# Kernel optimization log

Hardware: AMD Instinct MI355X
Metric: run time of the kernel (lower is better)

The kernel has to match this reference:

```python
import jax, jax.numpy as jnp
import numpy as np

DIM = 2048
HID = 1024
E = 16
TOP_K = 2
S_SHARED = 2


def setup_inputs() -> dict:
    key = jax.random.key(0)
    ks = jax.random.split(key, 6)
    scale = 0.02
    x = jax.random.normal(ks[0], (2, 2048, DIM), dtype=jnp.float32)
    gate_w = jax.random.normal(ks[1], (DIM, E), dtype=jnp.float32) * scale
    shared_w1 = jax.random.normal(ks[2], (S_SHARED, DIM, HID), dtype=jnp.float32) * scale
    shared_w2 = jax.random.normal(ks[3], (S_SHARED, HID, DIM), dtype=jnp.float32) * scale
    w1 = jax.random.normal(ks[4], (E, DIM, HID), dtype=jnp.float32) * scale
    w2 = jax.random.normal(ks[5], (E, HID, DIM), dtype=jnp.float32) * scale
    return {"x": x, "gate_w": gate_w, "shared_w1": shared_w1,
            "shared_w2": shared_w2, "w1": w1, "w2": w2}


def reference(x, gate_w, shared_w1, shared_w2, w1, w2):
    orig_shape = x.shape
    xf = x.reshape(-1, orig_shape[-1])  # [T, D]

    # Shared experts: sum of SiLU MLPs
    hs = jax.nn.silu(jnp.einsum('td,sdh->sth', xf, shared_w1))
    shared_out = jnp.einsum('sth,shd->td', hs, shared_w2)

    # Gating
    probs = jax.nn.softmax(xf @ gate_w, axis=-1)              # [T, E]
    weights, indices = jax.lax.top_k(probs, TOP_K)            # [T, K]
    weights = weights / weights.sum(axis=-1, keepdims=True)
    aux_loss = (probs.mean(axis=0) ** 2).sum() * E

    # Combine weights per (token, expert): top_k indices are distinct
    combine = (jax.nn.one_hot(indices, E, dtype=xf.dtype) *
               weights[..., None]).sum(axis=1)                # [T, E]

    # Dense all-expert compute (reference form of gather-GEMM-scatter)
    h = jax.nn.silu(jnp.einsum('td,edh->eth', xf, w1))        # [E, T, H]
    y = jnp.einsum('eth,ehd->etd', h, w2)                     # [E, T, D]
    routed_out = jnp.einsum('te,etd->td', combine, y)         # [T, D]

    out = (shared_out + routed_out).reshape(orig_shape)
    return out, aux_loss
```

## Files before the change

### kernel.cpp

```cpp
#include <hip/hip_runtime.h>
#include <math.h>

typedef unsigned short u16;
typedef __bf16 bf16x8 __attribute__((ext_vector_type(8)));
typedef float f32x4 __attribute__((ext_vector_type(4)));
typedef unsigned short u16x8 __attribute__((ext_vector_type(8)));

#define T_TOK 4096
#define DIMD 2048
#define HIDD 1024
#define NEXP 16
#define RMAX 10240
#define MAXBLK 96
#define BM 128
#define BN 256
#define BK 64

__device__ __forceinline__ u16 f2b(float f) {
  unsigned u = __builtin_bit_cast(unsigned, f);
  unsigned r = (u + 0x7FFFu + ((u >> 16) & 1u)) >> 16;
  return (u16)r;
}

__device__ __forceinline__ void gld16(const void* g, void* l) {
  __builtin_amdgcn_global_load_lds(
      (const __attribute__((address_space(1))) void*)g,
      (__attribute__((address_space(3))) void*)l, 16, 0, 0);
}


__global__ void k_pre(const float* __restrict__ x, u16* __restrict__ xb,
                      float* __restrict__ out, int* __restrict__ perm,
                      int* __restrict__ cnt, int* __restrict__ fill) {
  const int i = blockIdx.x * blockDim.x + threadIdx.x;
  const float4 v = ((const float4*)x)[i];
  union { u16 u[4]; unsigned long long q; } t;
  t.u[0] = f2b(v.x); t.u[1] = f2b(v.y); t.u[2] = f2b(v.z); t.u[3] = f2b(v.w);
  ((unsigned long long*)xb)[i] = t.q;
  float4 z = {0.f, 0.f, 0.f, 0.f};
  ((float4*)out)[i] = z;
  if (i < RMAX) perm[i] = -1;
  if (i < NEXP) { cnt[i] = 0; fill[i] = 0; }
}

template <int ID>
__global__ __launch_bounds__(256)
void k_tr2(const float* __restrict__ W, u16* __restrict__ Wt,
           int K, int N, long estride, int ld_out) {
  __shared__ float t[64][65];
  const int e = blockIdx.z;
  const float* Win = W + (size_t)e * (size_t)K * (size_t)N;
  u16* Wo = Wt + (size_t)e * (size_t)estride;
  const int n0 = blockIdx.x * 64, k0 = blockIdx.y * 64;
  {
    const int r = threadIdx.x >> 4;
    const int c = (threadIdx.x & 15) * 4;
#pragma unroll
    for (int p = 0; p < 4; ++p) {
      const int kk = p * 16 + r;
      const float4 v = *(const float4*)&Win[(size_t)(k0 + kk) * N + n0 + c];
      t[kk][c] = v.x; t[kk][c + 1] = v.y; t[kk][c + 2] = v.z; t[kk][c + 3] = v.w;
    }
  }
  __syncthreads();
  {
    const int r2 = threadIdx.x >> 3;
    const int g8 = (threadIdx.x & 7) * 8;
#pragma unroll
    for (int p = 0; p < 2; ++p) {
      const int nn = p * 32 + r2;
      u16x8 o;
#pragma unroll
      for (int i = 0; i < 8; ++i) o[i] = f2b(t[g8 + i][nn]);
      *(u16x8*)&Wo[(size_t)(n0 + nn) * ld_out + k0 + g8] = o;
    }
  }
}

__global__ __launch_bounds__(256)
void k_gate(const float* __restrict__ x, const float* __restrict__ gw,
            int* __restrict__ top2i, float* __restrict__ top2w,
            int* __restrict__ cnt, float* __restrict__ partial) {
  const int e = threadIdx.x & 15;
  const int tt = threadIdx.x >> 4;
  const int t = blockIdx.x * 16 + tt;
  const float* xp = x + (size_t)t * DIMD;
  float acc = 0.f;
#pragma unroll 8
  for (int k = 0; k < DIMD; ++k) acc = fmaf(xp[k], gw[k * NEXP + e], acc);
  __shared__ float lg[16][17];
  __shared__ float pr[16][17];
  lg[tt][e] = acc;
  __syncthreads();
  if (e == 0) {
    float l[16];
    float mx = -1e30f;
    for (int j = 0; j < 16; ++j) { l[j] = lg[tt][j]; mx = fmaxf(mx, l[j]); }
    float s = 0.f;
    for (int j = 0; j < 16; ++j) { l[j] = expf(l[j] - mx); s += l[j]; }
    const float inv = 1.f / s;
    float p1 = -1.f, p2 = -1.f; int i1 = 0, i2 = 0;
    for (int j = 0; j < 16; ++j) {
      const float p = l[j] * inv;
      pr[tt][j] = p;
      if (p > p1) { p2 = p1; i2 = i1; p1 = p; i1 = j; }
      else if (p > p2) { p2 = p; i2 = j; }
    }
    const float wsum = p1 + p2;
    top2i[t * 2 + 0] = i1;
    top2i[t * 2 + 1] = i2;
    top2w[t * 2 + 0] = p1 / wsum;
    top2w[t * 2 + 1] = p2 / wsum;
    atomicAdd(&cnt[i1], 1);
    atomicAdd(&cnt[i2], 1);
  }
  __syncthreads();
  if (tt == 0) {
    float s = 0.f;
    for (int j = 0; j < 16; ++j) s += pr[j][e];
    partial[blockIdx.x * 16 + e] = s;
  }
}

__global__ __launch_bounds__(256)
void k_aux(const float* __restrict__ partial, float* __restrict__ auxOut) {
  __shared__ float s[16][17];
  const int e = threadIdx.x & 15, c = threadIdx.x >> 4;
  float a = 0.f;
  for (int b = c; b < 256; b += 16) a += partial[b * 16 + e];
  s[c][e] = a;
  __syncthreads();
  if (threadIdx.x == 0) {
    float aux = 0.f;
    for (int j = 0; j < 16; ++j) {
      float tot = 0.f;
      for (int cc = 0; cc < 16; ++cc) tot += s[cc][j];
      const float m = tot / (float)T_TOK;
      aux += m * m;
    }
    auxOut[0] = aux * (float)NEXP;
  }
}

__global__ void k_off(const int* __restrict__ cnt, int* __restrict__ offs,
                      int* __restrict__ tbl_e, int* __restrict__ tbl_r0,
                      int* __restrict__ nblk) {
  if (threadIdx.x != 0 || blockIdx.x != 0) return;
  int o = 0, nb = 0;
  for (int e = 0; e < NEXP; ++e) {
    offs[e] = o;
    const int b = (cnt[e] + BM - 1) / BM;
    for (int i = 0; i < b; ++i) { tbl_e[nb] = e; tbl_r0[nb] = o + i * BM; ++nb; }
    o += b * BM;
  }
  offs[NEXP] = o;
  nblk[0] = nb;
}

__global__ void k_fill(const int* __restrict__ top2i, const float* __restrict__ top2w,
                       const int* __restrict__ offs, int* __restrict__ fill,
                       int* __restrict__ perm, float* __restrict__ wrow) {
  const int id = blockIdx.x * blockDim.x + threadIdx.x;
  if (id >= T_TOK * 2) return;
  const int e = top2i[id];
  const int pos = atomicAdd(&fill[e], 1);
  const int r = offs[e] + pos;
  perm[r] = id >> 1;
  wrow[r] = top2w[id];
}


__device__ __forceinline__ void stage_tile(
    const u16* gA0, const u16* gA1, const u16* gB0, const u16* gB1,
    const u16* gB2, const u16* gB3, int k0, u16* S, int b, int w) {
  u16* As = S + b * 24576;
  u16* Bs = As + 8192;
  gld16(gA0 + k0, As + w * 512);
  gld16(gA1 + k0, As + 4096 + w * 512);
  gld16(gB0 + k0, Bs + w * 512);
  gld16(gB1 + k0, Bs + 4096 + w * 512);
  gld16(gB2 + k0, Bs + 8192 + w * 512);
  gld16(gB3 + k0, Bs + 12288 + w * 512);
}

__device__ __forceinline__ void comp_tile(const u16* __restrict__ S, int b,
    const int (&aoff)[4][2], const int (&boff)[4][2], f32x4 (&acc)[4][4]) {
  const u16* As = S + b * 24576;
  const u16* Bs = As + 8192;
#pragma unroll
  for (int kh = 0; kh < 2; ++kh) {
    bf16x8 a[4], bq[4];
#pragma unroll
    for (int i = 0; i < 4; ++i) a[i] = *(const bf16x8*)(As + aoff[i][kh]);
#pragma unroll
    for (int j = 0; j < 4; ++j) bq[j] = *(const bf16x8*)(Bs + boff[j][kh]);
    __builtin_amdgcn_s_setprio(1);
#pragma unroll
    for (int i = 0; i < 4; ++i)
#pragma unroll
      for (int j = 0; j < 4; ++j)
        acc[i][j] = __builtin_amdgcn_mfma_f32_16x16x32_bf16(a[i], bq[j], acc[i][j], 0, 0, 0);
    __builtin_amdgcn_s_setprio(0);
  }
}

#define FENCE asm volatile("" ::: "memory")
#define VMW6  asm volatile("s_waitcnt vmcnt(6)" ::: "memory")
#define VMW0  asm volatile("s_waitcnt vmcnt(0)" ::: "memory")

__device__ __forceinline__ void gemm_pipe(
    const u16* gA0, const u16* gA1, const u16* gB0, const u16* gB1,
    const u16* gB2, const u16* gB3, int K, u16* S,
    const int (&aoff)[4][2], const int (&boff)[4][2],
    f32x4 (&acc)[4][4], int w) {
  const int nt = K >> 6;
  stage_tile(gA0, gA1, gB0, gB1, gB2, gB3, 0, S, 0, w);
  stage_tile(gA0, gA1, gB0, gB1, gB2, gB3, 64, S, 1, w);
  VMW6;
  __builtin_amdgcn_s_barrier();
  FENCE;
  for (int t = 0; t < nt - 2; ++t) {
    comp_tile(S, t & 1, aoff, boff, acc);
    FENCE;
    __builtin_amdgcn_s_barrier();
    FENCE;
    stage_tile(gA0, gA1, gB0, gB1, gB2, gB3, (t + 2) << 6, S, t & 1, w);
    VMW6;
    __builtin_amdgcn_s_barrier();
    FENCE;
  }
  comp_tile(S, 0, aoff, boff, acc);
  VMW0;
  __builtin_amdgcn_s_barrier();
  FENCE;
  comp_tile(S, 1, aoff, boff, acc);
}

__global__ __launch_bounds__(512, 2)
void k_up(const u16* __restrict__ xb, const u16* __restrict__ sw1t,
          const u16* __restrict__ w1t, u16* __restrict__ hbS,
          u16* __restrict__ hbR, const int* __restrict__ perm,
          const int* __restrict__ tbl_e, const int* __restrict__ tbl_r0,
          const int* __restrict__ nblk) {
  __shared__ u16 S[49152];
  const int bx = blockIdx.x, by = blockIdx.y;
  const int tid = threadIdx.x;
  const int w = tid >> 6, lane = tid & 63;
  const int lm = lane & 15, lq = lane >> 4;
  const int wm = w >> 2, wn = w & 3;
  const int srow = w * 8 + (lane >> 3);
  const int c8 = lane & 7;

  const bool routed = bx >= 32;
  int r0, ga0, ga1;
  const u16* Bb;
  if (!routed) {
    r0 = bx * BM;
    Bb = sw1t;
    ga0 = r0 + srow; ga1 = r0 + 64 + srow;
  } else {
    if (by >= 4) return;
    const int rbx = bx - 32;
    if (rbx >= *nblk) return;
    const int e = tbl_e[rbx];
    r0 = tbl_r0[rbx];
    Bb = w1t + (size_t)e * (size_t)HIDD * DIMD;
    const int p0 = perm[r0 + srow];      ga0 = (p0 < 0) ? 0 : p0;
    const int p1 = perm[r0 + 64 + srow]; ga1 = (p1 < 0) ? 0 : p1;
  }
  const int n0 = by * BN;
  const u16* gA0 = xb + (size_t)ga0 * DIMD + (c8 ^ ((srow >> 1) & 7)) * 8;
  const u16* gA1 = xb + (size_t)ga1 * DIMD + (c8 ^ (((64 + srow) >> 1) & 7)) * 8;
  const u16* gB[4];
#pragma unroll
  for (int p = 0; p < 4; ++p) {
    const int n = p * 64 + srow;
    gB[p] = Bb + (size_t)(n0 + n) * DIMD + (c8 ^ ((n >> 1) & 7)) * 8;
  }
  int aoff[4][2], boff[4][2];
#pragma unroll
  for (int i = 0; i < 4; ++i) {
    const int m = wm * 64 + i * 16 + lm;
    const int n = wn * 64 + i * 16 + lm;
#pragma unroll
    for (int kh = 0; kh < 2; ++kh) {
      aoff[i][kh] = m * 64 + (((kh << 2) | lq) ^ ((m >> 1) & 7)) * 8;
      boff[i][kh] = n * 64 + (((kh << 2) | lq) ^ ((n >> 1) & 7)) * 8;
    }
  }
  f32x4 acc[4][4];
#pragma unroll
  for (int i = 0; i < 4; ++i)
#pragma unroll
    for (int j = 0; j < 4; ++j) {
      acc[i][j][0] = 0.f; acc[i][j][1] = 0.f; acc[i][j][2] = 0.f; acc[i][j][3] = 0.f;
    }

  gemm_pipe(gA0, gA1, gB[0], gB[1], gB[2], gB[3], DIMD, S, aoff, boff, acc, w);

#pragma unroll
  for (int i = 0; i < 4; ++i) {
#pragma unroll
    for (int r = 0; r < 4; ++r) {
      const int row = r0 + wm * 64 + i * 16 + lq * 4 + r;
      u16* dst = routed ? &hbR[(size_t)row * HIDD] : &hbS[(size_t)row * DIMD];
#pragma unroll
      for (int j = 0; j < 4; ++j) {
        const int gc = n0 + wn * 64 + j * 16 + lm;
        const float v = acc[i][j][r];
        const float s = v / (1.f + expf(-v));
        dst[gc] = f2b(s);
      }
    }
  }
}

__global__ __launch_bounds__(512, 2)
void k_down(const u16* __restrict__ hbS, const u16* __restrict__ hbR,
            const u16* __restrict__ sw2ct, const u16* __restrict__ w2t,
            float* __restrict__ out, const int* __restrict__ perm,
            const float* __restrict__ wrow,
            const int* __restrict__ tbl_e, const int* __restrict__ tbl_r0,
            const int* __restrict__ nblk) {
  __shared__ u16 S[49152];
  const int bx = blockIdx.x, by = blockIdx.y;
  const int tid = threadIdx.x;
  const int w = tid >> 6, lane = tid & 63;
  const int lm = lane & 15, lq = lane >> 4;
  const int wm = w >> 2, wn = w & 3;
  const int srow = w * 8 + (lane >> 3);
  const int c8 = lane & 7;

  const bool routed = bx >= 32;
  int r0, K, ld;
  const u16 *Ab, *Bb;
  if (!routed) {
    r0 = bx * BM;
    Ab = hbS; K = DIMD; ld = DIMD;
    Bb = sw2ct;
  } else {
    const int rbx = bx - 32;
    if (rbx >= *nblk) return;
    const int e = tbl_e[rbx];
    r0 = tbl_r0[rbx];
    Ab = hbR; K = HIDD; ld = HIDD;
    Bb = w2t + (size_t)e * (size_t)DIMD * HIDD;
  }
  const int n0 = by * BN;
  const u16* gA0 = Ab + (size_t)(r0 + srow) * ld + (c8 ^ ((srow >> 1) & 7)) * 8;
  const u16* gA1 = Ab + (size_t)(r0 + 64 + srow) * ld + (c8 ^ (((64 + srow) >> 1) & 7)) * 8;
  const u16* gB[4];
#pragma unroll
  for (int p = 0; p < 4; ++p) {
    const int n = p * 64 + srow;
    gB[p] = Bb + (size_t)(n0 + n) * ld + (c8 ^ ((n >> 1) & 7)) * 8;
  }
  int aoff[4][2], boff[4][2];
#pragma unroll
  for (int i = 0; i < 4; ++i) {
    const int m = wm * 64 + i * 16 + lm;
    const int n = wn * 64 + i * 16 + lm;
#pragma unroll
    for (int kh = 0; kh < 2; ++kh) {
      aoff[i][kh] = m * 64 + (((kh << 2) | lq) ^ ((m >> 1) & 7)) * 8;
      boff[i][kh] = n * 64 + (((kh << 2) | lq) ^ ((n >> 1) & 7)) * 8;
    }
  }
  f32x4 acc[4][4];
#pragma unroll
  for (int i = 0; i < 4; ++i)
#pragma unroll
    for (int j = 0; j < 4; ++j) {
      acc[i][j][0] = 0.f; acc[i][j][1] = 0.f; acc[i][j][2] = 0.f; acc[i][j][3] = 0.f;
    }

  gemm_pipe(gA0, gA1, gB[0], gB[1], gB[2], gB[3], K, S, aoff, boff, acc, w);

#pragma unroll
  for (int i = 0; i < 4; ++i) {
#pragma unroll
    for (int r = 0; r < 4; ++r) {
      const int rr = r0 + wm * 64 + i * 16 + lq * 4 + r;
      int t; float wt;
      if (!routed) { t = rr; wt = 1.f; }
      else { t = perm[rr]; wt = (t >= 0) ? wrow[rr] : 0.f; }
      if (t >= 0) {
        float* dst = &out[(size_t)t * DIMD];
#pragma unroll
        for (int j = 0; j < 4; ++j) {
          const int gc = n0 + wn * 64 + j * 16 + lm;
          atomicAdd(&dst[gc], wt * acc[i][j][r]);
        }
      }
    }
  }
}


extern "C" void kernel_launch(void* const* d_in, const int* in_sizes, int n_in,
                              void* d_out, int out_size, void* d_ws, size_t ws_size,
                              hipStream_t stream) {
  const float* x   = (const float*)d_in[0];
  const float* gw  = (const float*)d_in[1];
  const float* sw1 = (const float*)d_in[2];
  const float* sw2 = (const float*)d_in[3];
  const float* w1  = (const float*)d_in[4];
  const float* w2  = (const float*)d_in[5];
  float* out = (float*)d_out;

  char* ws = (char*)d_ws;
  u16* xb    = (u16*)(ws);
  u16* hbS   = (u16*)(ws + (size_t)( 16 << 20));
  u16* hbR   = (u16*)(ws + (size_t)( 32 << 20));
  u16* sw1t  = (u16*)(ws + (size_t)( 56 << 20));
  u16* sw2ct = (u16*)(ws + (size_t)( 64 << 20));
  u16* w1t   = (u16*)(ws + (size_t)( 72 << 20));
  u16* w2t   = (u16*)(ws + (size_t)(136 << 20));
  char* p = ws + (size_t)(200 << 20);
  int*   top2i   = (int*)p;    p += T_TOK * 2 * 4;
  float* top2w   = (float*)p;  p += T_TOK * 2 * 4;
  int*   perm    = (int*)p;    p += RMAX * 4;
  float* wrow    = (float*)p;  p += RMAX * 4;
  int*   cnt     = (int*)p;    p += 16 * 4;
  int*   fill    = (int*)p;    p += 16 * 4;
  int*   offs    = (int*)p;    p += 32 * 4;
  int*   tbl_e   = (int*)p;    p += MAXBLK * 4;
  int*   tbl_r0  = (int*)p;    p += MAXBLK * 4;
  int*   nblk    = (int*)p;    p += 16 * 4;
  float* partial = (float*)p;  p += 256 * 16 * 4;

  k_pre<<<(T_TOK * DIMD / 4) / 256, 256, 0, stream>>>(x, xb, out, perm, cnt, fill);
  k_gate<<<T_TOK / 16, 256, 0, stream>>>(x, gw, top2i, top2w, cnt, partial);
  k_off<<<1, 64, 0, stream>>>(cnt, offs, tbl_e, tbl_r0, nblk);
  k_fill<<<(T_TOK * 2 + 255) / 256, 256, 0, stream>>>(top2i, top2w, offs, fill, perm, wrow);
  k_aux<<<1, 256, 0, stream>>>(partial, out + (size_t)T_TOK * DIMD);

  k_tr2<0><<<dim3(16, 32,  2), 256, 0, stream>>>(sw1, sw1t, 2048, 1024, 1024l * 2048, 2048);
  k_tr2<1><<<dim3(32, 16,  2), 256, 0, stream>>>(sw2, sw2ct, 1024, 2048, 1024, 2048);
  k_tr2<2><<<dim3(16, 32, 16), 256, 0, stream>>>(w1, w1t, 2048, 1024, 1024l * 2048, 2048);
  k_tr2<3><<<dim3(32, 16, 16), 256, 0, stream>>>(w2, w2t, 1024, 2048, 2048l * 1024, 1024);

  k_up<<<dim3(32 + MAXBLK, 8), 512, 0, stream>>>(xb, sw1t, w1t, hbS, hbR,
                                                 perm, tbl_e, tbl_r0, nblk);
  k_down<<<dim3(32 + MAXBLK, 8), 512, 0, stream>>>(hbS, hbR, sw2ct, w2t, out,
                                                   perm, wrow, tbl_e, tbl_r0, nblk);
}
```

Measured before the change: 806.5 us.

## Replace down-proj atomics with staged outputs and merge scheduling and transpose kernels

The down-projection kernel now writes the shared-expert output directly into `out` and the routed-expert rows into fp32 staging buffers. A new `k_post` kernel gathers each token's two routed rows and combines them with their weights, replacing per-element global atomicAdds. The routing-offset, fill and aux-loss kernels are merged into a single `k_sched` block, and the four weight-transpose launches become one launch. This also removes the zeroing of `out`. The trade-off is roughly 80MB of extra staging-buffer traffic, held in workspace regions reused from buffers that are no longer needed (xb and w1t), plus one extra launch.

After: 762.7 us. 1.06x faster.

```diff
diff --git a/kernel.cpp b/kernel.cpp
--- a/kernel.cpp
+++ b/kernel.cpp
@@ -30,51 +30,14 @@
 
 
 __global__ void k_pre(const float* __restrict__ x, u16* __restrict__ xb,
-                      float* __restrict__ out, int* __restrict__ perm,
-                      int* __restrict__ cnt, int* __restrict__ fill) {
+                      int* __restrict__ perm, int* __restrict__ cnt) {
   const int i = blockIdx.x * blockDim.x + threadIdx.x;
   const float4 v = ((const float4*)x)[i];
   union { u16 u[4]; unsigned long long q; } t;
   t.u[0] = f2b(v.x); t.u[1] = f2b(v.y); t.u[2] = f2b(v.z); t.u[3] = f2b(v.w);
   ((unsigned long long*)xb)[i] = t.q;
-  float4 z = {0.f, 0.f, 0.f, 0.f};
-  ((float4*)out)[i] = z;
   if (i < RMAX) perm[i] = -1;
-  if (i < NEXP) { cnt[i] = 0; fill[i] = 0; }
-}
-
-template <int ID>
-__global__ __launch_bounds__(256)
-void k_tr2(const float* __restrict__ W, u16* __restrict__ Wt,
-           int K, int N, long estride, int ld_out) {
-  __shared__ float t[64][65];
-  const int e = blockIdx.z;
-  const float* Win = W + (size_t)e * (size_t)K * (size_t)N;
-  u16* Wo = Wt + (size_t)e * (size_t)estride;
-  const int n0 = blockIdx.x * 64, k0 = blockIdx.y * 64;
-  {
-    const int r = threadIdx.x >> 4;
-    const int c = (threadIdx.x & 15) * 4;
-#pragma unroll
-    for (int p = 0; p < 4; ++p) {
-      const int kk = p * 16 + r;
-      const float4 v = *(const float4*)&Win[(size_t)(k0 + kk) * N + n0 + c];
-      t[kk][c] = v.x; t[kk][c + 1] = v.y; t[kk][c + 2] = v.z; t[kk][c + 3] = v.w;
-    }
-  }
-  __syncthreads();
-  {
-    const int r2 = threadIdx.x >> 3;
-    const int g8 = (threadIdx.x & 7) * 8;
-#pragma unroll
-    for (int p = 0; p < 2; ++p) {
-      const int nn = p * 32 + r2;
-      u16x8 o;
-#pragma unroll
-      for (int i = 0; i < 8; ++i) o[i] = f2b(t[g8 + i][nn]);
-      *(u16x8*)&Wo[(size_t)(n0 + nn) * ld_out + k0 + g8] = o;
-    }
-  }
+  if (i < NEXP) cnt[i] = 0;
 }
 
 __global__ __launch_bounds__(256)
@@ -123,14 +86,43 @@
 }
 
 __global__ __launch_bounds__(256)
-void k_aux(const float* __restrict__ partial, float* __restrict__ auxOut) {
+void k_sched(const int* __restrict__ cnt, const int* __restrict__ top2i,
+             const float* __restrict__ top2w, const float* __restrict__ partial,
+             int* __restrict__ tbl_e, int* __restrict__ tbl_r0,
+             int* __restrict__ nblk, int* __restrict__ perm,
+             float* __restrict__ wrow, int* __restrict__ slot2,
+             float* __restrict__ auxOut) {
+  __shared__ int offs[17];
+  __shared__ int lfill[16];
   __shared__ float s[16][17];
-  const int e = threadIdx.x & 15, c = threadIdx.x >> 4;
+  const int tid = threadIdx.x;
+  if (tid == 0) {
+    int o = 0, nb = 0;
+    for (int e = 0; e < NEXP; ++e) {
+      offs[e] = o;
+      const int b = (cnt[e] + BM - 1) / BM;
+      for (int i = 0; i < b; ++i) { tbl_e[nb] = e; tbl_r0[nb] = o + i * BM; ++nb; }
+      o += b * BM;
+    }
+    offs[16] = o;
+    nblk[0] = nb;
+  }
+  if (tid < 16) lfill[tid] = 0;
+  __syncthreads();
+  for (int id = tid; id < T_TOK * 2; id += 256) {
+    const int e = top2i[id];
+    const int pos = atomicAdd(&lfill[e], 1);
+    const int r = offs[e] + pos;
+    perm[r] = id >> 1;
+    wrow[r] = top2w[id];
+    slot2[id] = r;
+  }
+  const int e = tid & 15, c = tid >> 4;
   float a = 0.f;
   for (int b = c; b < 256; b += 16) a += partial[b * 16 + e];
   s[c][e] = a;
   __syncthreads();
-  if (threadIdx.x == 0) {
+  if (tid == 0) {
     float aux = 0.f;
     for (int j = 0; j < 16; ++j) {
       float tot = 0.f;
@@ -142,31 +134,78 @@
   }
 }
 
-__global__ void k_off(const int* __restrict__ cnt, int* __restrict__ offs,
-                      int* __restrict__ tbl_e, int* __restrict__ tbl_r0,
-                      int* __restrict__ nblk) {
-  if (threadIdx.x != 0 || blockIdx.x != 0) return;
-  int o = 0, nb = 0;
-  for (int e = 0; e < NEXP; ++e) {
-    offs[e] = o;
-    const int b = (cnt[e] + BM - 1) / BM;
-    for (int i = 0; i < b; ++i) { tbl_e[nb] = e; tbl_r0[nb] = o + i * BM; ++nb; }
-    o += b * BM;
-  }
-  offs[NEXP] = o;
-  nblk[0] = nb;
-}
-
-__global__ void k_fill(const int* __restrict__ top2i, const float* __restrict__ top2w,
-                       const int* __restrict__ offs, int* __restrict__ fill,
-                       int* __restrict__ perm, float* __restrict__ wrow) {
-  const int id = blockIdx.x * blockDim.x + threadIdx.x;
-  if (id >= T_TOK * 2) return;
-  const int e = top2i[id];
-  const int pos = atomicAdd(&fill[e], 1);
-  const int r = offs[e] + pos;
-  perm[r] = id >> 1;
-  wrow[r] = top2w[id];
+__global__ __launch_bounds__(256)
+void k_trW(const float* __restrict__ w1, const float* __restrict__ w2,
+           const float* __restrict__ sw1, const float* __restrict__ sw2,
+           u16* __restrict__ w1t, u16* __restrict__ w2t,
+           u16* __restrict__ sw1t, u16* __restrict__ sw2ct) {
+  const int z = blockIdx.z;
+  const float* W; u16* Wo; int K, N, ldo;
+  if (z < 16) {
+    W = w1 + (size_t)z * 2048 * 1024;
+    Wo = w1t + (size_t)z * 1024 * 2048;
+    K = 2048; N = 1024; ldo = 2048;
+  } else if (z < 32) {
+    W = w2 + (size_t)(z - 16) * 1024 * 2048;
+    Wo = w2t + (size_t)(z - 16) * 2048 * 1024;
+    K = 1024; N = 2048; ldo = 1024;
+  } else if (z < 34) {
+    W = sw1 + (size_t)(z - 32) * 2048 * 1024;
+    Wo = sw1t + (size_t)(z - 32) * 1024 * 2048;
+    K = 2048; N = 1024; ldo = 2048;
+  } else {
+    W = sw2 + (size_t)(z - 34) * 1024 * 2048;
+    Wo = sw2ct + (size_t)(z - 34) * 1024;
+    K = 1024; N = 2048; ldo = 2048;
+  }
+  const int n0 = blockIdx.x * 64, k0 = blockIdx.y * 64;
+  if (n0 >= N || k0 >= K) return;
+  __shared__ float t[64][65];
+  {
+    const int r = threadIdx.x >> 4;
+    const int c = (threadIdx.x & 15) * 4;
+#pragma unroll
+    for (int p = 0; p < 4; ++p) {
+      const int kk = p * 16 + r;
+      const float4 v = *(const float4*)&W[(size_t)(k0 + kk) * N + n0 + c];
+      t[kk][c] = v.x; t[kk][c + 1] = v.y; t[kk][c + 2] = v.z; t[kk][c + 3] = v.w;
+    }
+  }
+  __syncthreads();
+  {
+    const int r2 = threadIdx.x >> 3;
+    const int g8 = (threadIdx.x & 7) * 8;
+#pragma unroll
+    for (int p = 0; p < 2; ++p) {
+      const int nn = p * 32 + r2;
+      u16x8 o;
+#pragma unroll
+      for (int i = 0; i < 8; ++i) o[i] = f2b(t[g8 + i][nn]);
+      *(u16x8*)&Wo[(size_t)(n0 + nn) * ldo + k0 + g8] = o;
+    }
+  }
+}
+
+__global__ __launch_bounds__(512)
+void k_post(float* __restrict__ out, const float* __restrict__ rbLo,
+            const float* __restrict__ rbHi, const int* __restrict__ slot2,
+            const float* __restrict__ wrow) {
+  const int t = blockIdx.x;
+  const int d4 = threadIdx.x;
+  const int s0 = slot2[t * 2], s1 = slot2[t * 2 + 1];
+  const float w0 = wrow[s0], w1 = wrow[s1];
+  const float4* r0 = (const float4*)(s0 < 8192 ? rbLo + (size_t)s0 * DIMD
+                                               : rbHi + (size_t)(s0 - 8192) * DIMD);
+  const float4* r1 = (const float4*)(s1 < 8192 ? rbLo + (size_t)s1 * DIMD
+                                               : rbHi + (size_t)(s1 - 8192) * DIMD);
+  float4* op = (float4*)(out + (size_t)t * DIMD);
+  float4 o = op[d4];
+  const float4 a = r0[d4], b = r1[d4];
+  o.x += w0 * a.x + w1 * b.x;
+  o.y += w0 * a.y + w1 * b.y;
+  o.z += w0 * a.z + w1 * b.z;
+  o.w += w0 * a.w + w1 * b.w;
+  op[d4] = o;
 }
 
 
@@ -318,10 +357,9 @@
 __global__ __launch_bounds__(512, 2)
 void k_down(const u16* __restrict__ hbS, const u16* __restrict__ hbR,
             const u16* __restrict__ sw2ct, const u16* __restrict__ w2t,
-            float* __restrict__ out, const int* __restrict__ perm,
-            const float* __restrict__ wrow,
-            const int* __restrict__ tbl_e, const int* __restrict__ tbl_r0,
-            const int* __restrict__ nblk) {
+            float* __restrict__ out, float* __restrict__ rbLo,
+            float* __restrict__ rbHi, const int* __restrict__ tbl_e,
+            const int* __restrict__ tbl_r0, const int* __restrict__ nblk) {
   __shared__ u16 S[49152];
   const int bx = blockIdx.x, by = blockIdx.y;
   const int tid = threadIdx.x;
@@ -381,16 +419,14 @@
 #pragma unroll
     for (int r = 0; r < 4; ++r) {
       const int rr = r0 + wm * 64 + i * 16 + lq * 4 + r;
-      int t; float wt;
-      if (!routed) { t = rr; wt = 1.f; }
-      else { t = perm[rr]; wt = (t >= 0) ? wrow[rr] : 0.f; }
-      if (t >= 0) {
-        float* dst = &out[(size_t)t * DIMD];
-#pragma unroll
-        for (int j = 0; j < 4; ++j) {
-          const int gc = n0 + wn * 64 + j * 16 + lm;
-          atomicAdd(&dst[gc], wt * acc[i][j][r]);
-        }
+      float* dst;
+      if (!routed) dst = out + (size_t)rr * DIMD;
+      else dst = (rr < 8192) ? rbLo + (size_t)rr * DIMD
+                             : rbHi + (size_t)(rr - 8192) * DIMD;
+#pragma unroll
+      for (int j = 0; j < 4; ++j) {
+        const int gc = n0 + wn * 64 + j * 16 + lm;
+        dst[gc] = acc[i][j][r];
       }
     }
   }
@@ -416,32 +452,30 @@
   u16* sw2ct = (u16*)(ws + (size_t)( 64 << 20));
   u16* w1t   = (u16*)(ws + (size_t)( 72 << 20));
   u16* w2t   = (u16*)(ws + (size_t)(136 << 20));
+  float* rbLo = (float*)(ws + (size_t)( 72 << 20));
+  float* rbHi = (float*)(ws);
   char* p = ws + (size_t)(200 << 20);
   int*   top2i   = (int*)p;    p += T_TOK * 2 * 4;
   float* top2w   = (float*)p;  p += T_TOK * 2 * 4;
   int*   perm    = (int*)p;    p += RMAX * 4;
   float* wrow    = (float*)p;  p += RMAX * 4;
+  int*   slot2   = (int*)p;    p += T_TOK * 2 * 4;
   int*   cnt     = (int*)p;    p += 16 * 4;
-  int*   fill    = (int*)p;    p += 16 * 4;
-  int*   offs    = (int*)p;    p += 32 * 4;
   int*   tbl_e   = (int*)p;    p += MAXBLK * 4;
   int*   tbl_r0  = (int*)p;    p += MAXBLK * 4;
   int*   nblk    = (int*)p;    p += 16 * 4;
   float* partial = (float*)p;  p += 256 * 16 * 4;
 
-  k_pre<<<(T_TOK * DIMD / 4) / 256, 256, 0, stream>>>(x, xb, out, perm, cnt, fill);
+  k_pre<<<(T_TOK * DIMD / 4) / 256, 256, 0, stream>>>(x, xb, perm, cnt);
   k_gate<<<T_TOK / 16, 256, 0, stream>>>(x, gw, top2i, top2w, cnt, partial);
-  k_off<<<1, 64, 0, stream>>>(cnt, offs, tbl_e, tbl_r0, nblk);
-  k_fill<<<(T_TOK * 2 + 255) / 256, 256, 0, stream>>>(top2i, top2w, offs, fill, perm, wrow);
-  k_aux<<<1, 256, 0, stream>>>(partial, out + (size_t)T_TOK * DIMD);
-
-  k_tr2<0><<<dim3(16, 32,  2), 256, 0, stream>>>(sw1, sw1t, 2048, 1024, 1024l * 2048, 2048);
-  k_tr2<1><<<dim3(32, 16,  2), 256, 0, stream>>>(sw2, sw2ct, 1024, 2048, 1024, 2048);
-  k_tr2<2><<<dim3(16, 32, 16), 256, 0, stream>>>(w1, w1t, 2048, 1024, 1024l * 2048, 2048);
-  k_tr2<3><<<dim3(32, 16, 16), 256, 0, stream>>>(w2, w2t, 1024, 2048, 2048l * 1024, 1024);
-
+  k_sched<<<1, 256, 0, stream>>>(cnt, top2i, top2w, partial, tbl_e, tbl_r0,
+                                 nblk, perm, wrow, slot2,
+                                 out + (size_t)T_TOK * DIMD);
+  k_trW<<<dim3(32, 32, 36), 256, 0, stream>>>(w1, w2, sw1, sw2,
+                                              w1t, w2t, sw1t, sw2ct);
   k_up<<<dim3(32 + MAXBLK, 8), 512, 0, stream>>>(xb, sw1t, w1t, hbS, hbR,
                                                  perm, tbl_e, tbl_r0, nblk);
   k_down<<<dim3(32 + MAXBLK, 8), 512, 0, stream>>>(hbS, hbR, sw2ct, w2t, out,
-                                                   perm, wrow, tbl_e, tbl_r0, nblk);
-}
+                                                   rbLo, rbHi, tbl_e, tbl_r0, nblk);
+  k_post<<<T_TOK, 512, 0, stream>>>(out, rbLo, rbHi, slot2, wrow);
+}
```
